# Optimization experiments

Measured on AMD Instinct MI355X. Metric: run time of the kernel, lower is better.

Reference implementation:

```python
import jax, jax.numpy as jnp
import numpy as np

B, S, E, H = 2, 2048, 512, 8
D = E // H  # head size = 64
LN_EPS = 1e-5


def setup_inputs() -> dict:
    key = jax.random.key(0)
    ks = jax.random.split(key, 8)
    s_in = 1.0 / np.sqrt(E)
    return {
        "x": jax.random.normal(ks[0], (B, S, E), jnp.float32),
        # per-head projection weights, stored [H, E, D] so q = x @ Wq[h]
        "Wq": jax.random.normal(ks[1], (H, E, D), jnp.float32) * s_in,
        "Wk": jax.random.normal(ks[2], (H, E, D), jnp.float32) * s_in,
        "Wv": jax.random.normal(ks[3], (H, E, D), jnp.float32) * s_in,
        "Wp": jax.random.normal(ks[4], (E, E), jnp.float32) * s_in,
        "bp": jnp.zeros((E,), jnp.float32),
        "gamma": jnp.ones((E,), jnp.float32),
        "beta": jnp.zeros((E,), jnp.float32),
        # causal mask buffer: masked_fill where mask == 0
        "mask": jnp.tril(jnp.ones((S, S), jnp.int32)),
    }


def reference(x, Wq, Wk, Wv, Wp, bp, gamma, beta, mask):
    # batched per-head projections (equivalent to the H small Linears)
    q = jnp.einsum("bse,hed->bhsd", x, Wq)
    k = jnp.einsum("bse,hed->bhsd", x, Wk)
    v = jnp.einsum("bse,hed->bhsd", x, Wv)
    # NOTE: original has NO 1/sqrt(d) scaling
    att_log = jnp.einsum("bhsd,bhtd->bhst", q, k)
    att_log = jnp.where(mask == 0, -jnp.inf, att_log)
    att = jax.nn.softmax(att_log, axis=-1)
    o = jnp.einsum("bhst,bhtd->bhsd", att, v)  # [B,H,S,D]
    # torch.cat((val, values)) prepends each head -> final order head H-1 .. 0
    o = o[:, ::-1]
    vals = o.transpose(0, 2, 1, 3).reshape(B, S, E)
    out = vals @ Wp.T + bp + x
    mu = jnp.mean(out, axis=-1, keepdims=True)
    var = jnp.var(out, axis=-1, keepdims=True)
    return (out - mu) * jax.lax.rsqrt(var + LN_EPS) * gamma + beta
```

## Files before the change

kernel.cpp:

```cpp
#include <hip/hip_runtime.h>

constexpr int Bn = 2;
constexpr int Sn = 2048;
constexpr int En = 512;
constexpr int Hn = 8;
constexpr int Dn = 64;
constexpr int Mn = Bn * Sn;

typedef short bf8 __attribute__((ext_vector_type(8)));
typedef float f32x4 __attribute__((ext_vector_type(4)));

constexpr size_t XY = (size_t)Mn * En;
constexpr size_t WT = (size_t)3 * En * En;
constexpr size_t WP = (size_t)En * En;
constexpr size_t PL = (size_t)Bn * Hn * Sn * Dn;

__device__ __forceinline__ unsigned short f2bf(float f) {
    unsigned int u = __float_as_uint(f);
    unsigned int r = 0x7FFFu + ((u >> 16) & 1u);
    return (unsigned short)((u + r) >> 16);
}
__device__ __forceinline__ float bf2f(unsigned short u) {
    return __uint_as_float(((unsigned int)u) << 16);
}
__device__ __forceinline__ void split2(float f, unsigned short& hi, unsigned short& lo) {
    hi = f2bf(f);
    lo = f2bf(f - bf2f(hi));
}

__global__ __launch_bounds__(256)
void prep(const float* __restrict__ x, const float* __restrict__ Wp,
          const float* __restrict__ Wq, const float* __restrict__ Wk,
          const float* __restrict__ Wv,
          unsigned short* __restrict__ xh, unsigned short* __restrict__ xl,
          unsigned short* __restrict__ Wph, unsigned short* __restrict__ Wpl,
          unsigned short* __restrict__ Wth, unsigned short* __restrict__ Wtl)
{
    __shared__ float t[64][65];
    const int bid = blockIdx.x;
    const int tid = threadIdx.x;

    if (bid < 1152) {
        const float* src = (bid < 1024) ? x : Wp;
        unsigned short* hp = (bid < 1024) ? xh : Wph;
        unsigned short* lp = (bid < 1024) ? xl : Wpl;
        const int blk = (bid < 1024) ? bid : (bid - 1024);
        const size_t base = ((size_t)blk * 256 + tid) * 8;
        float a[8];
        *(float4*)&a[0] = *(const float4*)(src + base);
        *(float4*)&a[4] = *(const float4*)(src + base + 4);
        unsigned short h[8], l[8];
        #pragma unroll
        for (int j = 0; j < 8; ++j) split2(a[j], h[j], l[j]);
        *(bf8*)(hp + base) = *(bf8*)&h[0];
        *(bf8*)(lp + base) = *(bf8*)&l[0];
        return;
    }

    const int idx = bid - 1152;
    const int ph = idx >> 3;
    const int proj = ph >> 3, h = ph & 7;
    const int e0 = (idx & 7) * 64;
    const float* W = (proj == 0) ? Wq : (proj == 1) ? Wk : Wv;
    const float* src = W + (size_t)h * En * Dn + (size_t)e0 * Dn;

    const int er = tid >> 2, cg = (tid & 3) * 16;
    #pragma unroll
    for (int c = 0; c < 4; ++c) {
        float4 v = *(const float4*)(src + (size_t)er * Dn + cg + 4 * c);
        t[er][cg + 4 * c + 0] = v.x;
        t[er][cg + 4 * c + 1] = v.y;
        t[er][cg + 4 * c + 2] = v.z;
        t[er][cg + 4 * c + 3] = v.w;
    }
    __syncthreads();

    const int d = tid >> 2, jg = (tid & 3) * 16;
    unsigned short h16[16], l16[16];
    #pragma unroll
    for (int j = 0; j < 16; ++j) split2(t[jg + j][d], h16[j], l16[j]);
    const size_t n = (size_t)proj * 512 + h * 64 + d;
    unsigned short* dh = Wth + n * En + e0 + jg;
    unsigned short* dl = Wtl + n * En + e0 + jg;
    *(bf8*)dh       = *(bf8*)&h16[0];
    *(bf8*)(dh + 8) = *(bf8*)&h16[8];
    *(bf8*)dl       = *(bf8*)&l16[0];
    *(bf8*)(dl + 8) = *(bf8*)&l16[8];
}

__global__ __launch_bounds__(256)
void qkv_gemm(const unsigned short* __restrict__ xh,
              const unsigned short* __restrict__ xl,
              const unsigned short* __restrict__ Wth,
              const unsigned short* __restrict__ Wtl,
              unsigned short* __restrict__ qh_g,
              unsigned short* __restrict__ ql_g,
              unsigned short* __restrict__ kh_g,
              unsigned short* __restrict__ kl_g,
              unsigned short* __restrict__ vT_g)
{
    __shared__ __align__(16) unsigned char smraw[30720];
    unsigned short (*Ah)[40] = (unsigned short(*)[40])(smraw);
    unsigned short (*Al)[40] = (unsigned short(*)[40])(smraw + 10240);
    unsigned short (*Bh)[40] = (unsigned short(*)[40])(smraw + 20480);
    unsigned short (*Bl)[40] = (unsigned short(*)[40])(smraw + 25600);
    float (*Cf)[68] = (float(*)[68])(smraw);

    const int tid = threadIdx.x;
    const int m0 = blockIdx.x * 128;
    const int ny = blockIdx.y;
    const int proj = ny >> 3, h = ny & 7;

    const int wave = tid >> 6, lane = tid & 63;
    const int wm = (wave >> 1) * 64, wn = (wave & 1) * 32;
    const int lm = lane & 15, quad = lane >> 4;

    const int am = tid >> 1;
    const int aks = (tid & 1) * 16;
    const unsigned short* arh = xh + (size_t)(m0 + am) * En + aks;
    const unsigned short* arl = xl + (size_t)(m0 + am) * En + aks;

    const int bn = tid >> 2;
    const int bks = (tid & 3) * 8;
    const unsigned short* brh = Wth + (size_t)(ny * 64 + bn) * En + bks;
    const unsigned short* brl = Wtl + (size_t)(ny * 64 + bn) * En + bks;

    f32x4 acc[4][2];
    #pragma unroll
    for (int i = 0; i < 4; ++i)
        #pragma unroll
        for (int j = 0; j < 2; ++j) acc[i][j] = (f32x4){0.f, 0.f, 0.f, 0.f};

    for (int k0 = 0; k0 < En; k0 += 32) {
        *(bf8*)&Ah[am][aks]     = *(const bf8*)(arh + k0);
        *(bf8*)&Ah[am][aks + 8] = *(const bf8*)(arh + k0 + 8);
        *(bf8*)&Al[am][aks]     = *(const bf8*)(arl + k0);
        *(bf8*)&Al[am][aks + 8] = *(const bf8*)(arl + k0 + 8);
        *(bf8*)&Bh[bn][bks]     = *(const bf8*)(brh + k0);
        *(bf8*)&Bl[bn][bks]     = *(const bf8*)(brl + k0);
        __syncthreads();

        bf8 a_h[4], a_l[4], b_h[2], b_l[2];
        #pragma unroll
        for (int mi = 0; mi < 4; ++mi) {
            a_h[mi] = *(const bf8*)&Ah[wm + mi * 16 + lm][quad * 8];
            a_l[mi] = *(const bf8*)&Al[wm + mi * 16 + lm][quad * 8];
        }
        #pragma unroll
        for (int ni = 0; ni < 2; ++ni) {
            b_h[ni] = *(const bf8*)&Bh[wn + ni * 16 + lm][quad * 8];
            b_l[ni] = *(const bf8*)&Bl[wn + ni * 16 + lm][quad * 8];
        }
        #pragma unroll
        for (int mi = 0; mi < 4; ++mi)
            #pragma unroll
            for (int ni = 0; ni < 2; ++ni) {
                acc[mi][ni] = __builtin_amdgcn_mfma_f32_16x16x32_bf16(a_h[mi], b_h[ni], acc[mi][ni], 0, 0, 0);
                acc[mi][ni] = __builtin_amdgcn_mfma_f32_16x16x32_bf16(a_h[mi], b_l[ni], acc[mi][ni], 0, 0, 0);
                acc[mi][ni] = __builtin_amdgcn_mfma_f32_16x16x32_bf16(a_l[mi], b_h[ni], acc[mi][ni], 0, 0, 0);
            }
        __syncthreads();
    }

    if (proj < 2) {
        unsigned short* hp = (proj == 0) ? qh_g : kh_g;
        unsigned short* lp = (proj == 0) ? ql_g : kl_g;
        #pragma unroll
        for (int p = 0; p < 2; ++p) {
            if ((wave >> 1) == p) {
                #pragma unroll
                for (int mi = 0; mi < 4; ++mi)
                    #pragma unroll
                    for (int ni = 0; ni < 2; ++ni)
                        #pragma unroll
                        for (int r = 0; r < 4; ++r)
                            Cf[mi * 16 + quad * 4 + r][wn + ni * 16 + lm] = acc[mi][ni][r];
            }
            __syncthreads();
            {
                const int lr = tid & 63;
                const int cg = (tid >> 6) * 16;
                const int m = m0 + p * 64 + lr;
                const int b = m >> 11, s = m & 2047;
                unsigned short hi[16], lo[16];
                #pragma unroll
                for (int j4 = 0; j4 < 4; ++j4) {
                    float4 v = *(const float4*)&Cf[lr][cg + 4 * j4];
                    split2(v.x, hi[4 * j4 + 0], lo[4 * j4 + 0]);
                    split2(v.y, hi[4 * j4 + 1], lo[4 * j4 + 1]);
                    split2(v.z, hi[4 * j4 + 2], lo[4 * j4 + 2]);
                    split2(v.w, hi[4 * j4 + 3], lo[4 * j4 + 3]);
                }
                const size_t base = (((size_t)(b * Hn + h) * Sn + s) * Dn) + cg;
                *(bf8*)(hp + base)     = *(bf8*)&hi[0];
                *(bf8*)(hp + base + 8) = *(bf8*)&hi[8];
                *(bf8*)(lp + base)     = *(bf8*)&lo[0];
                *(bf8*)(lp + base + 8) = *(bf8*)&lo[8];
            }
            __syncthreads();
        }
    } else {
        #pragma unroll
        for (int mi = 0; mi < 4; ++mi) {
            const int s0 = m0 + wm + mi * 16 + quad * 4;
            const int b = s0 >> 11, s = s0 & 2047;
            #pragma unroll
            for (int ni = 0; ni < 2; ++ni) {
                const int d = wn + ni * 16 + lm;
                ushort4 pk;
                pk.x = f2bf(acc[mi][ni][0]);
                pk.y = f2bf(acc[mi][ni][1]);
                pk.z = f2bf(acc[mi][ni][2]);
                pk.w = f2bf(acc[mi][ni][3]);
                *(ushort4*)(vT_g + ((size_t)(b * Hn + h) * Dn + d) * Sn + s) = pk;
            }
        }
    }
}

__global__ __launch_bounds__(256)
void attn(const unsigned short* __restrict__ qh_g,
          const unsigned short* __restrict__ ql_g,
          const unsigned short* __restrict__ kh_g,
          const unsigned short* __restrict__ kl_g,
          const unsigned short* __restrict__ vT_g,
          unsigned short* __restrict__ Op,
          float* __restrict__ ml)
{
    extern __shared__ unsigned short sm[];
    unsigned short (*khs)[72] = (unsigned short(*)[72])(sm);
    unsigned short (*kls)[72] = (unsigned short(*)[72])(sm + 4608);
    unsigned short (*vTs)[72] = (unsigned short(*)[72])(sm + 9216);
    unsigned short (*pts)[72] = (unsigned short(*)[72])(sm + 13824);
    float* alf = (float*)(sm + 18432);

    const int bidx = blockIdx.x;
    const int r_ = bidx & 255, quarter = bidx >> 8;
    const int a_ = r_ >> 4, bh = r_ & 15;
    const int qt = (quarter & 1) ? (31 - a_) : a_;
    const int hf = quarter >> 1;
    const int n0 = (qt + 2) >> 1;
    const int its = hf ? n0 : 0;
    const int ite = hf ? (qt + 1) : n0;
    const int pslot = hf * 512 + bh * 32 + qt;

    const int tid = threadIdx.x;
    const int wave = tid >> 6, lane = tid & 63;
    const int quad = lane >> 4, lq = lane & 15;

    const unsigned short* khb = kh_g + (size_t)bh * Sn * Dn;
    const unsigned short* klb = kl_g + (size_t)bh * Sn * Dn;
    const unsigned short* vTb = vT_g + (size_t)bh * Dn * Sn;

    bf8 qfh[2], qfl[2];
    {
        const size_t qoff = ((size_t)bh * Sn + (size_t)qt * 64 + wave * 16 + lq) * Dn;
        #pragma unroll
        for (int c = 0; c < 2; ++c) {
            qfh[c] = *(const bf8*)(qh_g + qoff + c * 32 + quad * 8);
            qfl[c] = *(const bf8*)(ql_g + qoff + c * 32 + quad * 8);
        }
    }

    f32x4 accO[4];
    #pragma unroll
    for (int nj = 0; nj < 4; ++nj) accO[nj] = (f32x4){0.f, 0.f, 0.f, 0.f};
    float m = -1e30f, l = 0.f;

    const int srow = tid & 63;
    const int sdg  = tid >> 6;

    bf8 pk0, pk1, pl0, pl1, pv0, pv1;
    if (its < ite) {
        const int t0 = its * 64;
        const unsigned short* kr = khb + (size_t)(t0 + srow) * Dn + sdg * 16;
        const unsigned short* lr = klb + (size_t)(t0 + srow) * Dn + sdg * 16;
        const unsigned short* vr = vTb + (size_t)srow * Sn + t0 + sdg * 16;
        pk0 = *(const bf8*)(kr);  pk1 = *(const bf8*)(kr + 8);
        pl0 = *(const bf8*)(lr);  pl1 = *(const bf8*)(lr + 8);
        pv0 = *(const bf8*)(vr);  pv1 = *(const bf8*)(vr + 8);
    }

    for (int it = its; it < ite; ++it) {
        __syncthreads();
        *(bf8*)&khs[srow][sdg * 16]     = pk0;
        *(bf8*)&khs[srow][sdg * 16 + 8] = pk1;
        *(bf8*)&kls[srow][sdg * 16]     = pl0;
        *(bf8*)&kls[srow][sdg * 16 + 8] = pl1;
        *(bf8*)&vTs[srow][sdg * 16]     = pv0;
        *(bf8*)&vTs[srow][sdg * 16 + 8] = pv1;
        __syncthreads();

        if (it + 1 < ite) {
            const int t1 = (it + 1) * 64;
            const unsigned short* kr = khb + (size_t)(t1 + srow) * Dn + sdg * 16;
            const unsigned short* lr = klb + (size_t)(t1 + srow) * Dn + sdg * 16;
            const unsigned short* vr = vTb + (size_t)srow * Sn + t1 + sdg * 16;
            pk0 = *(const bf8*)(kr);  pk1 = *(const bf8*)(kr + 8);
            pl0 = *(const bf8*)(lr);  pl1 = *(const bf8*)(lr + 8);
            pv0 = *(const bf8*)(vr);  pv1 = *(const bf8*)(vr + 8);
        }

        f32x4 accS[4];
        #pragma unroll
        for (int mi = 0; mi < 4; ++mi) accS[mi] = (f32x4){0.f, 0.f, 0.f, 0.f};
        #pragma unroll
        for (int mi = 0; mi < 4; ++mi) {
            #pragma unroll
            for (int c = 0; c < 2; ++c) {
                bf8 ah = *(const bf8*)&khs[mi * 16 + lq][c * 32 + quad * 8];
                bf8 al = *(const bf8*)&kls[mi * 16 + lq][c * 32 + quad * 8];
                accS[mi] = __builtin_amdgcn_mfma_f32_16x16x32_bf16(ah, qfh[c], accS[mi], 0, 0, 0);
                accS[mi] = __builtin_amdgcn_mfma_f32_16x16x32_bf16(ah, qfl[c], accS[mi], 0, 0, 0);
                accS[mi] = __builtin_amdgcn_mfma_f32_16x16x32_bf16(al, qfh[c], accS[mi], 0, 0, 0);
            }
        }

        if (it == qt) {
            const int qrel = wave * 16 + lq;
            #pragma unroll
            for (int mi = 0; mi < 4; ++mi)
                #pragma unroll
                for (int r = 0; r < 4; ++r)
                    if (mi * 16 + quad * 4 + r > qrel) accS[mi][r] = -INFINITY;
        }

        float mt = -INFINITY;
        #pragma unroll
        for (int mi = 0; mi < 4; ++mi)
            #pragma unroll
            for (int r = 0; r < 4; ++r) mt = fmaxf(mt, accS[mi][r]);
        mt = fmaxf(mt, __shfl_xor(mt, 16));
        mt = fmaxf(mt, __shfl_xor(mt, 32));
        const float mnew = fmaxf(m, mt);
        const float alpha = __expf(m - mnew);
        float ls = 0.f;
        #pragma unroll
        for (int mi = 0; mi < 4; ++mi)
            #pragma unroll
            for (int r = 0; r < 4; ++r) {
                const float p = __expf(accS[mi][r] - mnew);
                accS[mi][r] = p;
                ls += p;
            }
        ls += __shfl_xor(ls, 16);
        ls += __shfl_xor(ls, 32);
        l = l * alpha + ls;
        m = mnew;

        #pragma unroll
        for (int mi = 0; mi < 4; ++mi) {
            ushort4 pk;
            pk.x = f2bf(accS[mi][0]);
            pk.y = f2bf(accS[mi][1]);
            pk.z = f2bf(accS[mi][2]);
            pk.w = f2bf(accS[mi][3]);
            *(ushort4*)&pts[wave * 16 + lq][mi * 16 + quad * 4] = pk;
        }
        if (quad == 0) alf[wave * 16 + lq] = alpha;

        {
            float4 al4 = *(const float4*)&alf[wave * 16 + quad * 4];
            #pragma unroll
            for (int nj = 0; nj < 4; ++nj) {
                accO[nj][0] *= al4.x;
                accO[nj][1] *= al4.y;
                accO[nj][2] *= al4.z;
                accO[nj][3] *= al4.w;
            }
            #pragma unroll
            for (int c = 0; c < 2; ++c) {
                bf8 pf = *(const bf8*)&pts[wave * 16 + lq][c * 32 + quad * 8];
                #pragma unroll
                for (int nj = 0; nj < 4; ++nj) {
                    bf8 vf = *(const bf8*)&vTs[nj * 16 + lq][c * 32 + quad * 8];
                    accO[nj] = __builtin_amdgcn_mfma_f32_16x16x32_bf16(pf, vf, accO[nj], 0, 0, 0);
                }
            }
        }
    }

    if (quad == 0) {
        const size_t mi_ = ((size_t)pslot * 64 + wave * 16 + lq) * 2;
        ml[mi_]     = m;
        ml[mi_ + 1] = l;
    }
    #pragma unroll
    for (int r = 0; r < 4; ++r) {
        const int q = wave * 16 + quad * 4 + r;
        unsigned short* dst = Op + ((size_t)pslot * 64 + q) * 64;
        #pragma unroll
        for (int nj = 0; nj < 4; ++nj)
            dst[nj * 16 + lq] = f2bf(accO[nj][r]);
    }
}

__global__ __launch_bounds__(256)
void out_gemm(const unsigned short* __restrict__ Op,
              const float* __restrict__ ml,
              const unsigned short* __restrict__ Wph,
              const unsigned short* __restrict__ Wpl,
              const float* __restrict__ bp,
              const float* __restrict__ x,
              float* __restrict__ outp,
              float* __restrict__ outp2)
{
    __shared__ unsigned short Ah[64][40], Al[64][40];
    __shared__ unsigned short Bh[128][40], Bl[128][40];

    const int tid = threadIdx.x;
    const int m0 = blockIdx.x * 64;
    const int n0 = blockIdx.y * 128;
    const int kz = blockIdx.z;
    const int kbeg = kz * 256, kend = kbeg + 256;

    const int wave = tid >> 6, lane = tid & 63;
    const int wm = (wave >> 1) * 32, wn = (wave & 1) * 64;
    const int lm = lane & 15, quad = lane >> 4;

    const int am = tid >> 2;
    const int aks = (tid & 3) * 8;
    const int m_row = m0 + am;
    const int b_row = m_row >> 11, s_row = m_row & 2047;
    const int qt = s_row >> 6, qq = s_row & 63;

    float c0[8], c1[8];
    #pragma unroll
    for (int h = 0; h < 8; ++h) {
        const size_t base0 = (((size_t)(b_row * 8 + h) * 32 + qt) * 64 + qq) * 2;
        const size_t base1 = base0 + (size_t)512 * 64 * 2;
        const float m0_ = ml[base0], l0_ = ml[base0 + 1];
        const float m1_ = ml[base1], l1_ = ml[base1 + 1];
        const float mn = fmaxf(m0_, m1_);
        const float a0 = __expf(m0_ - mn), a1 = __expf(m1_ - mn);
        const float inv = 1.f / (a0 * l0_ + a1 * l1_);
        c0[h] = a0 * inv;
        c1[h] = a1 * inv;
    }

    const int bn = tid >> 1;
    const int bks = (tid & 1) * 16;
    const unsigned short* brh = Wph + (size_t)(n0 + bn) * En + bks;
    const unsigned short* brl = Wpl + (size_t)(n0 + bn) * En + bks;

    f32x4 acc[2][4];
    #pragma unroll
    for (int i = 0; i < 2; ++i)
        #pragma unroll
        for (int j = 0; j < 4; ++j) acc[i][j] = (f32x4){0.f, 0.f, 0.f, 0.f};

    for (int k0 = kbeg; k0 < kend; k0 += 32) {
        {
            const int e0 = k0 + aks;
            const int h = 7 - (e0 >> 6);
            const int d = e0 & 63;
            const size_t p0 = (((size_t)(b_row * 8 + h) * 32 + qt) * 64 + qq) * 64 + d;
            const size_t p1 = p0 + (size_t)512 * 64 * 64;
            bf8 o0 = *(const bf8*)(Op + p0);
            bf8 o1 = *(const bf8*)(Op + p1);
            const float w0 = c0[h], w1 = c1[h];
            unsigned short hi[8], lo[8];
            #pragma unroll
            for (int j = 0; j < 8; ++j) {
                const float v = w0 * bf2f((unsigned short)o0[j]) +
                                w1 * bf2f((unsigned short)o1[j]);
                split2(v, hi[j], lo[j]);
            }
            *(bf8*)&Ah[am][aks] = *(bf8*)&hi[0];
            *(bf8*)&Al[am][aks] = *(bf8*)&lo[0];
        }
        *(bf8*)&Bh[bn][bks]     = *(const bf8*)(brh + k0);
        *(bf8*)&Bh[bn][bks + 8] = *(const bf8*)(brh + k0 + 8);
        *(bf8*)&Bl[bn][bks]     = *(const bf8*)(brl + k0);
        *(bf8*)&Bl[bn][bks + 8] = *(const bf8*)(brl + k0 + 8);
        __syncthreads();

        bf8 a_h[2], a_l[2], b_h[4], b_l[4];
        #pragma unroll
        for (int mi = 0; mi < 2; ++mi) {
            a_h[mi] = *(const bf8*)&Ah[wm + mi * 16 + lm][quad * 8];
            a_l[mi] = *(const bf8*)&Al[wm + mi * 16 + lm][quad * 8];
        }
        #pragma unroll
        for (int ni = 0; ni < 4; ++ni) {
            b_h[ni] = *(const bf8*)&Bh[wn + ni * 16 + lm][quad * 8];
            b_l[ni] = *(const bf8*)&Bl[wn + ni * 16 + lm][quad * 8];
        }
        #pragma unroll
        for (int mi = 0; mi < 2; ++mi)
            #pragma unroll
            for (int ni = 0; ni < 4; ++ni) {
                acc[mi][ni] = __builtin_amdgcn_mfma_f32_16x16x32_bf16(a_h[mi], b_h[ni], acc[mi][ni], 0, 0, 0);
                acc[mi][ni] = __builtin_amdgcn_mfma_f32_16x16x32_bf16(a_h[mi], b_l[ni], acc[mi][ni], 0, 0, 0);
                acc[mi][ni] = __builtin_amdgcn_mfma_f32_16x16x32_bf16(a_l[mi], b_h[ni], acc[mi][ni], 0, 0, 0);
            }
        __syncthreads();
    }

    float* dst = kz ? outp2 : outp;
    #pragma unroll
    for (int mi = 0; mi < 2; ++mi) {
        #pragma unroll
        for (int r = 0; r < 4; ++r) {
            const int m = m0 + wm + mi * 16 + quad * 4 + r;
            #pragma unroll
            for (int ni = 0; ni < 4; ++ni) {
                const int n = n0 + wn + ni * 16 + lm;
                const size_t idx = (size_t)m * En + n;
                const float extra = kz ? 0.f : (bp[n] + x[idx]);
                dst[idx] = acc[mi][ni][r] + extra;
            }
        }
    }
}

__global__ __launch_bounds__(256)
void ln_kernel(const float* __restrict__ outp,
               const float* __restrict__ outp2,
               const float* __restrict__ gamma,
               const float* __restrict__ beta,
               float* __restrict__ y)
{
    const int row = blockIdx.x * 4 + (threadIdx.x >> 6);
    const int lane = threadIdx.x & 63;
    const size_t off = (size_t)row * En + lane * 8;

    float a[8], b2[8];
    *(float4*)&a[0] = *(const float4*)(outp + off);
    *(float4*)&a[4] = *(const float4*)(outp + off + 4);
    *(float4*)&b2[0] = *(const float4*)(outp2 + off);
    *(float4*)&b2[4] = *(const float4*)(outp2 + off + 4);
    #pragma unroll
    for (int j = 0; j < 8; ++j) a[j] += b2[j];

    float sum = 0.f, sq = 0.f;
    #pragma unroll
    for (int j = 0; j < 8; ++j) { sum += a[j]; sq += a[j] * a[j]; }
    #pragma unroll
    for (int off_ = 1; off_ < 64; off_ <<= 1) {
        sum += __shfl_xor(sum, off_);
        sq  += __shfl_xor(sq, off_);
    }
    const float mu = sum * (1.f / 512.f);
    const float var = sq * (1.f / 512.f) - mu * mu;
    const float rs = rsqrtf(var + 1e-5f);

    const float* g = gamma + lane * 8;
    const float* be = beta + lane * 8;
    float o[8];
    #pragma unroll
    for (int j = 0; j < 8; ++j)
        o[j] = (a[j] - mu) * rs * g[j] + be[j];
    float* yr = y + off;
    *(float4*)(yr)     = *(float4*)&o[0];
    *(float4*)(yr + 4) = *(float4*)&o[4];
}

extern "C" void kernel_launch(void* const* d_in, const int* in_sizes, int n_in,
                              void* d_out, int out_size, void* d_ws, size_t ws_size,
                              hipStream_t stream)
{
    const float* x     = (const float*)d_in[0];
    const float* Wq    = (const float*)d_in[1];
    const float* Wk    = (const float*)d_in[2];
    const float* Wv    = (const float*)d_in[3];
    const float* Wp    = (const float*)d_in[4];
    const float* bp    = (const float*)d_in[5];
    const float* gamma = (const float*)d_in[6];
    const float* beta  = (const float*)d_in[7];

    float* ws   = (float*)d_ws;
    float* ml   = ws;
    float* outp = ws + XY;
    unsigned short* bfb = (unsigned short*)(ws + 2 * XY);
    unsigned short* xh  = bfb;
    unsigned short* xl  = bfb + XY;
    unsigned short* Wth = bfb + 2 * XY;
    unsigned short* Wtl = Wth + WT;
    unsigned short* Wph = Wtl + WT;
    unsigned short* Wpl = Wph + WP;
    unsigned short* qh  = Wpl + WP;
    unsigned short* ql  = qh + PL;
    unsigned short* kh  = ql + PL;
    unsigned short* kl  = kh + PL;
    unsigned short* vT  = kl + PL;
    unsigned short* Op = xh;
    float* outp2 = (float*)qh;

    const int attn_lds = 18432 * 2 + 256;
    hipFuncSetAttribute((const void*)attn,
                        hipFuncAttributeMaxDynamicSharedMemorySize, attn_lds);

    prep<<<dim3(1344), 256, 0, stream>>>(x, Wp, Wq, Wk, Wv,
                                         xh, xl, Wph, Wpl, Wth, Wtl);
    qkv_gemm<<<dim3(Mn / 128, 24), 256, 0, stream>>>(xh, xl, Wth, Wtl,
                                                     qh, ql, kh, kl, vT);
    attn<<<dim3(1024), 256, attn_lds, stream>>>(qh, ql, kh, kl, vT, Op, ml);
    out_gemm<<<dim3(Mn / 64, En / 128, 2), 256, 0, stream>>>(Op, ml, Wph, Wpl,
                                                             bp, x, outp, outp2);
    ln_kernel<<<dim3(Mn / 4), 256, 0, stream>>>(outp, outp2, gamma, beta,
                                                (float*)d_out);
}
```

Measured before the change: 178.4 us.

## Split attention KV range into four partitions per query tile

Each query tile's key/value range is now split four ways instead of two, which doubles the number of attention blocks to 2048. The aim is better load balance and more occupancy across the GPU. The output GEMM merges the four partial results using their stored max and sum statistics. This costs more partial-output traffic and extra merge work in out_gemm, and the workspace buffers are remapped to hold the extra partials.

```diff
diff --git a/kernel.cpp b/kernel.cpp
--- a/kernel.cpp
+++ b/kernel.cpp
@@ -224,7 +224,10 @@
           const unsigned short* __restrict__ kh_g,
           const unsigned short* __restrict__ kl_g,
           const unsigned short* __restrict__ vT_g,
-          unsigned short* __restrict__ Op,
+          unsigned short* __restrict__ Op0,
+          unsigned short* __restrict__ Op1,
+          unsigned short* __restrict__ Op2,
+          unsigned short* __restrict__ Op3,
           float* __restrict__ ml)
 {
     extern __shared__ unsigned short sm[];
@@ -235,14 +238,14 @@
     float* alf = (float*)(sm + 18432);
 
     const int bidx = blockIdx.x;
-    const int r_ = bidx & 255, quarter = bidx >> 8;
+    const int j4 = bidx >> 9;
+    const int r_ = bidx & 511;
     const int a_ = r_ >> 4, bh = r_ & 15;
-    const int qt = (quarter & 1) ? (31 - a_) : a_;
-    const int hf = quarter >> 1;
-    const int n0 = (qt + 2) >> 1;
-    const int its = hf ? n0 : 0;
-    const int ite = hf ? (qt + 1) : n0;
-    const int pslot = hf * 512 + bh * 32 + qt;
+    const int qt = (j4 & 1) ? (31 - a_) : a_;
+    const int its = ((qt + 1) * j4) >> 2;
+    const int ite = ((qt + 1) * (j4 + 1)) >> 2;
+    const int pslot = j4 * 512 + bh * 32 + qt;
+    unsigned short* Opj = (j4 == 0) ? Op0 : (j4 == 1) ? Op1 : (j4 == 2) ? Op2 : Op3;
 
     const int tid = threadIdx.x;
     const int wave = tid >> 6, lane = tid & 63;
@@ -388,7 +391,7 @@
     #pragma unroll
     for (int r = 0; r < 4; ++r) {
         const int q = wave * 16 + quad * 4 + r;
-        unsigned short* dst = Op + ((size_t)pslot * 64 + q) * 64;
+        unsigned short* dst = Opj + (((size_t)(bh * 32 + qt)) * 64 + q) * 64;
         #pragma unroll
         for (int nj = 0; nj < 4; ++nj)
             dst[nj * 16 + lq] = f2bf(accO[nj][r]);
@@ -396,7 +399,10 @@
 }
 
 __global__ __launch_bounds__(256)
-void out_gemm(const unsigned short* __restrict__ Op,
+void out_gemm(const unsigned short* __restrict__ Op0,
+              const unsigned short* __restrict__ Op1,
+              const unsigned short* __restrict__ Op2,
+              const unsigned short* __restrict__ Op3,
               const float* __restrict__ ml,
               const unsigned short* __restrict__ Wph,
               const unsigned short* __restrict__ Wpl,
@@ -424,18 +430,24 @@
     const int b_row = m_row >> 11, s_row = m_row & 2047;
     const int qt = s_row >> 6, qq = s_row & 63;
 
-    float c0[8], c1[8];
+    float cw[8][4];
     #pragma unroll
     for (int h = 0; h < 8; ++h) {
-        const size_t base0 = (((size_t)(b_row * 8 + h) * 32 + qt) * 64 + qq) * 2;
-        const size_t base1 = base0 + (size_t)512 * 64 * 2;
-        const float m0_ = ml[base0], l0_ = ml[base0 + 1];
-        const float m1_ = ml[base1], l1_ = ml[base1 + 1];
-        const float mn = fmaxf(m0_, m1_);
-        const float a0 = __expf(m0_ - mn), a1 = __expf(m1_ - mn);
-        const float inv = 1.f / (a0 * l0_ + a1 * l1_);
-        c0[h] = a0 * inv;
-        c1[h] = a1 * inv;
+        const int slot = (b_row * 8 + h) * 32 + qt;
+        float mj[4], lj[4];
+        #pragma unroll
+        for (int j = 0; j < 4; ++j) {
+            const size_t base = (((size_t)(j * 512 + slot)) * 64 + qq) * 2;
+            mj[j] = ml[base];
+            lj[j] = ml[base + 1];
+        }
+        float mn = fmaxf(fmaxf(mj[0], mj[1]), fmaxf(mj[2], mj[3]));
+        float aj[4], denom = 0.f;
+        #pragma unroll
+        for (int j = 0; j < 4; ++j) { aj[j] = __expf(mj[j] - mn); denom += aj[j] * lj[j]; }
+        const float inv = 1.f / denom;
+        #pragma unroll
+        for (int j = 0; j < 4; ++j) cw[h][j] = aj[j] * inv;
     }
 
     const int bn = tid >> 1;
@@ -454,16 +466,19 @@
             const int e0 = k0 + aks;
             const int h = 7 - (e0 >> 6);
             const int d = e0 & 63;
-            const size_t p0 = (((size_t)(b_row * 8 + h) * 32 + qt) * 64 + qq) * 64 + d;
-            const size_t p1 = p0 + (size_t)512 * 64 * 64;
-            bf8 o0 = *(const bf8*)(Op + p0);
-            bf8 o1 = *(const bf8*)(Op + p1);
-            const float w0 = c0[h], w1 = c1[h];
+            const size_t po = (((size_t)((b_row * 8 + h) * 32 + qt)) * 64 + qq) * 64 + d;
+            bf8 o0 = *(const bf8*)(Op0 + po);
+            bf8 o1 = *(const bf8*)(Op1 + po);
+            bf8 o2 = *(const bf8*)(Op2 + po);
+            bf8 o3 = *(const bf8*)(Op3 + po);
+            const float w0 = cw[h][0], w1 = cw[h][1], w2 = cw[h][2], w3 = cw[h][3];
             unsigned short hi[8], lo[8];
             #pragma unroll
             for (int j = 0; j < 8; ++j) {
                 const float v = w0 * bf2f((unsigned short)o0[j]) +
-                                w1 * bf2f((unsigned short)o1[j]);
+                                w1 * bf2f((unsigned short)o1[j]) +
+                                w2 * bf2f((unsigned short)o2[j]) +
+                                w3 * bf2f((unsigned short)o3[j]);
                 split2(v, hi[j], lo[j]);
             }
             *(bf8*)&Ah[am][aks] = *(bf8*)&hi[0];
@@ -569,9 +584,10 @@
     const float* gamma = (const float*)d_in[6];
     const float* beta  = (const float*)d_in[7];
 
-    float* ws   = (float*)d_ws;
-    float* ml   = ws;
-    float* outp = ws + XY;
+    float* ws = (float*)d_ws;
+    float* ml = ws;
+    unsigned short* Op2 = (unsigned short*)(ws + 262144);
+    unsigned short* Op3 = (unsigned short*)(ws + XY);
     unsigned short* bfb = (unsigned short*)(ws + 2 * XY);
     unsigned short* xh  = bfb;
     unsigned short* xl  = bfb + XY;
@@ -584,8 +600,10 @@
     unsigned short* kh  = ql + PL;
     unsigned short* kl  = kh + PL;
     unsigned short* vT  = kl + PL;
-    unsigned short* Op = xh;
-    float* outp2 = (float*)qh;
+    unsigned short* Op0 = xh;
+    unsigned short* Op1 = xl;
+    float* outp  = (float*)qh;
+    float* outp2 = (float*)kh;
 
     const int attn_lds = 18432 * 2 + 256;
     hipFuncSetAttribute((const void*)attn,
@@ -595,8 +613,10 @@
                                          xh, xl, Wph, Wpl, Wth, Wtl);
     qkv_gemm<<<dim3(Mn / 128, 24), 256, 0, stream>>>(xh, xl, Wth, Wtl,
                                                      qh, ql, kh, kl, vT);
-    attn<<<dim3(1024), 256, attn_lds, stream>>>(qh, ql, kh, kl, vT, Op, ml);
-    out_gemm<<<dim3(Mn / 64, En / 128, 2), 256, 0, stream>>>(Op, ml, Wph, Wpl,
+    attn<<<dim3(2048), 256, attn_lds, stream>>>(qh, ql, kh, kl, vT,
+                                                Op0, Op1, Op2, Op3, ml);
+    out_gemm<<<dim3(Mn / 64, En / 128, 2), 256, 0, stream>>>(Op0, Op1, Op2, Op3,
+                                                             ml, Wph, Wpl,
                                                              bp, x, outp, outp2);
     ln_kernel<<<dim3(Mn / 4), 256, 0, stream>>>(outp, outp2, gamma, beta,
                                                 (float*)d_out);
```

New measurement: 185.1 us. 1.04x slower.
